# Kernel tuning notes

Measured on AMD Instinct MI355X. Metric: run time of the kernel, lower is better.

The kernel has to match this reference:

```python
import jax, jax.numpy as jnp
import numpy as np

VOCAB = 100000
EMB = 256
HID = 512
HH = HID // 2  # per-direction hidden
NTAGS = 12
START = 10
STOP = 11
SEQ = 2048
NEG = -10000.0


def setup_inputs() -> dict:
    key = jax.random.key(0)
    ks = jax.random.split(key, 18)
    s = 0.05
    inp = {
        "sentence": jax.random.randint(ks[0], (SEQ,), 0, VOCAB, dtype=jnp.int64 if jax.config.jax_enable_x64 else jnp.int32),
        "tags": jax.random.randint(ks[1], (SEQ,), 0, 10, dtype=jnp.int64 if jax.config.jax_enable_x64 else jnp.int32),
        "embed": jax.random.normal(ks[2], (VOCAB, EMB), jnp.float32) * s,
        "Wih_f": jax.random.normal(ks[3], (4 * HH, EMB), jnp.float32) * s,
        "Whh_f": jax.random.normal(ks[4], (4 * HH, HH), jnp.float32) * s,
        "bih_f": jax.random.normal(ks[5], (4 * HH,), jnp.float32) * s,
        "bhh_f": jax.random.normal(ks[6], (4 * HH,), jnp.float32) * s,
        "Wih_b": jax.random.normal(ks[7], (4 * HH, EMB), jnp.float32) * s,
        "Whh_b": jax.random.normal(ks[8], (4 * HH, HH), jnp.float32) * s,
        "bih_b": jax.random.normal(ks[9], (4 * HH,), jnp.float32) * s,
        "bhh_b": jax.random.normal(ks[10], (4 * HH,), jnp.float32) * s,
        "W_out": jax.random.normal(ks[11], (NTAGS, HID), jnp.float32) * s,
        "b_out": jax.random.normal(ks[12], (NTAGS,), jnp.float32) * s,
        "h0": jax.random.normal(ks[14], (2, HH), jnp.float32),
        "c0": jax.random.normal(ks[15], (2, HH), jnp.float32),
    }
    trans = jax.random.normal(ks[13], (NTAGS, NTAGS), jnp.float32)
    trans = trans.at[START, :].set(NEG)  # never transition INTO start
    trans = trans.at[:, STOP].set(NEG)   # never transition FROM stop
    inp["transitions"] = trans
    return inp


def _lstm_dir(x, h0, c0, Wih, Whh, bih, bhh):
    # x: [T, E]; PyTorch gate order i, f, g, o
    pre = x @ Wih.T + bih + bhh  # [T, 4*HH] precomputed input projection
    def step(carry, p):
        h, c = carry
        g = p + Whh @ h
        i, f, gg, o = jnp.split(g, 4)
        i = jax.nn.sigmoid(i)
        f = jax.nn.sigmoid(f)
        gg = jnp.tanh(gg)
        o = jax.nn.sigmoid(o)
        c = f * c + i * gg
        h = o * jnp.tanh(c)
        return (h, c), h
    _, hs = jax.lax.scan(step, (h0, c0), pre)
    return hs  # [T, HH]


def _forward_impl(sentence, tags, embed, Wih_f, Whh_f, bih_f, bhh_f,
                  Wih_b, Whh_b, bih_b, bhh_b, W_out, b_out, transitions, h0, c0):
    x = embed[sentence]  # [T, E]
    hf = _lstm_dir(x, h0[0], c0[0], Wih_f, Whh_f, bih_f, bhh_f)
    hb = jnp.flip(_lstm_dir(jnp.flip(x, 0), h0[1], c0[1], Wih_b, Whh_b, bih_b, bhh_b), 0)
    feats = jnp.concatenate([hf, hb], axis=-1) @ W_out.T + b_out  # [T, NTAGS]

    # CRF forward algorithm: log-semiring scan over time
    fv0 = jnp.full((NTAGS,), NEG, feats.dtype).at[START].set(0.0)
    def crf_step(fv, emit):
        # transitions[next, prev]; logsumexp over prev
        fv = jax.nn.logsumexp(fv[None, :] + transitions + emit[:, None], axis=1)
        return fv, None
    fv, _ = jax.lax.scan(crf_step, fv0, feats)
    forward_score = jax.nn.logsumexp(fv + transitions[STOP])

    # gold path score
    prev = jnp.concatenate([jnp.array([START], dtype=tags.dtype), tags[:-1]])
    emit_gold = jnp.take_along_axis(feats, tags[:, None], axis=1)[:, 0]
    gold_score = jnp.sum(transitions[tags, prev]) + jnp.sum(emit_gold) + transitions[STOP, tags[-1]]

    return forward_score - gold_score


def reference(sentence, tags, embed, Wih_f, Whh_f, bih_f, bhh_f,
              Wih_b, Whh_b, bih_b, bhh_b, W_out, b_out, transitions, h0, c0):
    return _forward_impl(sentence, tags, embed, Wih_f, Whh_f, bih_f, bhh_f,
                         Wih_b, Whh_b, bih_b, bhh_b, W_out, b_out, transitions, h0, c0)
```

## Files before the change

### kernel.cpp

```cpp
#include <hip/hip_runtime.h>
#include <hip/hip_bf16.h>
#include <stdint.h>

#define SEQ   2048
#define EMB   256
#define HHD   256
#define GATES 1024
#define NTAGS 12
#define START 10
#define STOP  11
#define CCH   16
#define CLEN  128

__device__ __forceinline__ int sdot4(uint32_t a, uint32_t b, int c) {
#if __has_builtin(__builtin_amdgcn_sdot4)
  return __builtin_amdgcn_sdot4((int)a, (int)b, c, false);
#else
  int r = c;
#pragma unroll
  for (int i = 0; i < 4; i++) {
    int av = (int)(signed char)((a >> (8 * i)) & 255);
    int bv = (int)(signed char)((b >> (8 * i)) & 255);
    r += av * bv;
  }
  return r;
#endif
}

__device__ __forceinline__ float fsig(float x) {
  float e = __expf(-x);
  return __builtin_amdgcn_rcpf(1.0f + e);
}

__device__ __forceinline__ int dpp_xor1(int x) {
  return __builtin_amdgcn_update_dpp(0, x, 0xB1, 0xF, 0xF, true);
}
__device__ __forceinline__ int dpp_xor2(int x) {
  return __builtin_amdgcn_update_dpp(0, x, 0x4E, 0xF, 0xF, true);
}
__device__ __forceinline__ float dpp_xor2_f(float x) {
  int r = __builtin_amdgcn_update_dpp(0, __float_as_int(x), 0x4E, 0xF, 0xF, true);
  return __int_as_float(r);
}

__global__ __launch_bounds__(256) void k_quant(const float* __restrict__ whh_f,
                                               const float* __restrict__ whh_b,
                                               uint32_t* __restrict__ q4,
                                               float* __restrict__ scales) {
  const int row  = (blockIdx.x * 256 + threadIdx.x) >> 6;
  const int lane = threadIdx.x & 63;
  const int d = row >> 10, r = row & 1023;
  const float4 w = *(const float4*)((d ? whh_b : whh_f) + (long)r * HHD + lane * 4);
  float m = fmaxf(fmaxf(fabsf(w.x), fabsf(w.y)), fmaxf(fabsf(w.z), fabsf(w.w)));
#pragma unroll
  for (int off = 32; off; off >>= 1) m = fmaxf(m, __shfl_xor(m, off, 64));
  m = fmaxf(m, 1e-20f);
  const float inv = 127.f / m;
  int a = (int)rintf(w.x * inv), b = (int)rintf(w.y * inv);
  int c = (int)rintf(w.z * inv), e = (int)rintf(w.w * inv);
  q4[row * 64 + lane] = (uint32_t)(a & 255) | ((uint32_t)(b & 255) << 8) |
                        ((uint32_t)(c & 255) << 16) | ((uint32_t)(e & 255) << 24);
  if (lane == 0) scales[row] = m / 127.f;
}

__global__ __launch_bounds__(256) void k_proj(const int* __restrict__ sentence,
                                              const float* __restrict__ embed,
                                              const float* __restrict__ Wih_f,
                                              const float* __restrict__ bih_f,
                                              const float* __restrict__ bhh_f,
                                              const float* __restrict__ Wih_b,
                                              const float* __restrict__ bih_b,
                                              const float* __restrict__ bhh_b,
                                              float* __restrict__ pre) {
  const int dir = blockIdx.y;
  const int t0  = blockIdx.x * 8;
  const float* Wih = dir ? Wih_b : Wih_f;
  const float* bih = dir ? bih_b : bih_f;
  const float* bhh = dir ? bhh_b : bhh_f;

  __shared__ float xs[8][256];
  const int tid = threadIdx.x;
#pragma unroll
  for (int i = 0; i < 8; i++) {
    int s = sentence[t0 + i];
    xs[i][tid] = embed[(long)s * EMB + tid];
  }
  __syncthreads();

  const int r0 = tid * 4;
  float acc[4][8];
#pragma unroll
  for (int j = 0; j < 4; j++)
#pragma unroll
    for (int t = 0; t < 8; t++) acc[j][t] = 0.f;

  const float4* W4 = (const float4*)Wih;
  for (int kq = 0; kq < 64; kq++) {
    float4 w[4];
#pragma unroll
    for (int j = 0; j < 4; j++) w[j] = W4[(r0 + j) * 64 + kq];
#pragma unroll
    for (int t = 0; t < 8; t++) {
      float4 xv = ((const float4*)xs[t])[kq];
#pragma unroll
      for (int j = 0; j < 4; j++)
        acc[j][t] += w[j].x * xv.x + w[j].y * xv.y + w[j].z * xv.z + w[j].w * xv.w;
    }
  }
#pragma unroll
  for (int j = 0; j < 4; j++) {
    const int row = r0 + j;
    const int G  = row >> 8;
    const int uu = row & 255;
    float bsum = bih[row] + bhh[row];
#pragma unroll
    for (int t = 0; t < 8; t++)
      pre[(((long)(dir * SEQ + t0 + t)) * HHD + uu) * 4 + G] = acc[j][t] + bsum;
  }
}

__global__ __launch_bounds__(512, 2) void k_lstm(const uint32_t* __restrict__ q4,
                                                 const float* __restrict__ scales,
                                                 const float* __restrict__ pre,
                                                 const float* __restrict__ h0,
                                                 const float* __restrict__ c0,
                                                 float* __restrict__ hs) {
  const int dir  = blockIdx.x;
  const int L    = threadIdx.x;
  const int q    = L & 3;
  const int g    = L >> 2;
  const int p    = q & 1;
  const int half = q >> 1;
  const int u    = 2 * g + p;

  __shared__ __align__(16) uint8_t hbuf[2][256];

  const long base = (long)dir * GATES;

  uint4 wa[4][4], wb[4][4];
  const uint4* qq = (const uint4*)q4;
#pragma unroll
  for (int j = 0; j < 4; j++) {
    const int qj = q ^ j;
    const int rA = (2 * (qj >> 1)) * 256 + 2 * g + (qj & 1);
    const int rB = rA + 256;
#pragma unroll
    for (int k = 0; k < 4; k++) {
      wa[j][k] = qq[(base + rA) * 16 + 4 * q + k];
      wb[j][k] = qq[(base + rB) * 16 + 4 * q + k];
    }
  }
  const int rown = (2 * half) * 256 + u;
  const float sA = scales[base + rown];
  const float sB = scales[base + rown + 256];
  const float sA1 = sA * (1.f / 127.f), sA4 = sA * (4.f / 127.f);
  const float sB1 = sB * (1.f / 127.f), sB4 = sB * (4.f / 127.f);

  if (L < 256) {
    float v = h0[dir * HHD + L] * (127.f / 4.f);
    v = fminf(fmaxf(v, -127.f), 127.f);
    hbuf[0][L] = (uint8_t)(int)rintf(v);
  }
  float c_st = c0[dir * HHD + u];
  __syncthreads();

  const int t0 = dir ? (SEQ - 1) : 0;
  const long pstep = dir ? -(long)(HHD * 4) : (long)(HHD * 4);
  const long hstep = dir ? -(long)HHD : (long)HHD;
  const float* pp = pre + (long)dir * SEQ * (HHD * 4) + ((long)t0 * HHD + u) * 4 + 2 * half;
  float* hp       = hs  + (long)dir * SEQ * HHD + (long)t0 * HHD + u;
  const float gmul = half ? 2.f : 1.f;
  const int write_h = ((L & 2) == 0);

  float2 pr = *(const float2*)pp;

  for (int s = 0; s < SEQ; s++) {
#pragma unroll
    for (int j = 0; j < 4; j++)
#pragma unroll
      for (int k = 0; k < 4; k++) {
        asm volatile("" : "+v"(wa[j][k].x), "+v"(wa[j][k].y),
                          "+v"(wa[j][k].z), "+v"(wa[j][k].w));
        asm volatile("" : "+v"(wb[j][k].x), "+v"(wb[j][k].y),
                          "+v"(wb[j][k].z), "+v"(wb[j][k].w));
      }

    pp += pstep;
    const float2 prn = *(const float2*)pp;

    const uint4* hq4 = (const uint4*)(hbuf[s & 1] + (q << 6));
    const uint4 h0v = hq4[0], h1v = hq4[1], h2v = hq4[2], h3v = hq4[3];

    int pa0 = 0, pa1 = 0, pa2 = 0, pa3 = 0;
    int pb0 = 0, pb1 = 0, pb2 = 0, pb3 = 0;
#pragma unroll
    for (int k = 0; k < 4; k++) {
      const uint4 hk = (k == 0) ? h0v : (k == 1) ? h1v : (k == 2) ? h2v : h3v;
      pa0 = sdot4(wa[0][k].x, hk.x, pa0); pa0 = sdot4(wa[0][k].y, hk.y, pa0);
      pa0 = sdot4(wa[0][k].z, hk.z, pa0); pa0 = sdot4(wa[0][k].w, hk.w, pa0);
      pa1 = sdot4(wa[1][k].x, hk.x, pa1); pa1 = sdot4(wa[1][k].y, hk.y, pa1);
      pa1 = sdot4(wa[1][k].z, hk.z, pa1); pa1 = sdot4(wa[1][k].w, hk.w, pa1);
      pa2 = sdot4(wa[2][k].x, hk.x, pa2); pa2 = sdot4(wa[2][k].y, hk.y, pa2);
      pa2 = sdot4(wa[2][k].z, hk.z, pa2); pa2 = sdot4(wa[2][k].w, hk.w, pa2);
      pa3 = sdot4(wa[3][k].x, hk.x, pa3); pa3 = sdot4(wa[3][k].y, hk.y, pa3);
      pa3 = sdot4(wa[3][k].z, hk.z, pa3); pa3 = sdot4(wa[3][k].w, hk.w, pa3);
      pb0 = sdot4(wb[0][k].x, hk.x, pb0); pb0 = sdot4(wb[0][k].y, hk.y, pb0);
      pb0 = sdot4(wb[0][k].z, hk.z, pb0); pb0 = sdot4(wb[0][k].w, hk.w, pb0);
      pb1 = sdot4(wb[1][k].x, hk.x, pb1); pb1 = sdot4(wb[1][k].y, hk.y, pb1);
      pb1 = sdot4(wb[1][k].z, hk.z, pb1); pb1 = sdot4(wb[1][k].w, hk.w, pb1);
      pb2 = sdot4(wb[2][k].x, hk.x, pb2); pb2 = sdot4(wb[2][k].y, hk.y, pb2);
      pb2 = sdot4(wb[2][k].z, hk.z, pb2); pb2 = sdot4(wb[2][k].w, hk.w, pb2);
      pb3 = sdot4(wb[3][k].x, hk.x, pb3); pb3 = sdot4(wb[3][k].y, hk.y, pb3);
      pb3 = sdot4(wb[3][k].z, hk.z, pb3); pb3 = sdot4(wb[3][k].w, hk.w, pb3);
    }
    const int tA = pa0 + dpp_xor1(pa1);
    const int tA2 = pa2 + dpp_xor1(pa3);
    const int sumA = tA + dpp_xor2(tA2);
    const int tB = pb0 + dpp_xor1(pb1);
    const int tB2 = pb2 + dpp_xor1(pb3);
    const int sumB = tB + dpp_xor2(tB2);

    const float sAh = s ? sA1 : sA4;
    const float sBh = s ? sB1 : sB4;
    const float gA = fmaf(sAh, (float)sumA, pr.x);
    const float gB = fmaf(sBh, (float)sumB, pr.y);

    const float v0 = fsig(gA * gmul) * gmul - (gmul - 1.f);
    const float v1 = fsig(gB);
    const float p0 = dpp_xor2_f(v0);
    const float p1 = dpp_xor2_f(v1);
    const float iv = half ? p0 : v0;
    const float fv = half ? p1 : v1;
    const float gv = half ? v0 : p0;
    const float ov = half ? v1 : p1;

    c_st = fv * c_st + iv * gv;
    const float hv = ov * (2.f * fsig(2.f * c_st) - 1.f);

    if (write_h) {
      *hp = hv;
      hbuf[(s + 1) & 1][u] = (uint8_t)(int)rintf(hv * 127.f);
    }
    pr = prn;
    hp += hstep;
    asm volatile("s_waitcnt lgkmcnt(0)\n\ts_barrier" ::: "memory");
  }
}

__global__ __launch_bounds__(192) void k_feats(const float* __restrict__ hs,
                                               const float* __restrict__ W_out,
                                               const float* __restrict__ b_out,
                                               float* __restrict__ feats) {
  __shared__ float Wl[12 * 520];
  const int tid = threadIdx.x;
  for (int i = tid; i < 12 * 512; i += 192) Wl[(i / 512) * 520 + (i % 512)] = W_out[i];
  __syncthreads();

  const int tl = tid / 12, n = tid % 12;
  const int t = blockIdx.x * 16 + tl;
  const float4* hf4 = (const float4*)(hs + (long)t * HHD);
  const float4* hb4 = (const float4*)(hs + (long)SEQ * HHD + (long)t * HHD);
  const float4* Wa  = (const float4*)&Wl[n * 520];
  const float4* Wb  = (const float4*)&Wl[n * 520 + 256];

  float acc = b_out[n];
#pragma unroll 8
  for (int j = 0; j < 64; j++) {
    float4 w = Wa[j], h = hf4[j];
    acc += w.x * h.x + w.y * h.y + w.z * h.z + w.w * h.w;
  }
#pragma unroll 8
  for (int j = 0; j < 64; j++) {
    float4 w = Wb[j], h = hb4[j];
    acc += w.x * h.x + w.y * h.y + w.z * h.z + w.w * h.w;
  }
  feats[t * NTAGS + n] = acc;
}

__global__ __launch_bounds__(192) void k_crf_chunk(const float* __restrict__ feats,
                                                   const float* __restrict__ trans,
                                                   float* __restrict__ Pc) {
  const int ch  = blockIdx.x;
  const int tid = threadIdx.x;
  const int n   = tid & 15;
  const int p   = tid >> 4;
  const int nn  = (n < 12) ? n : 11;

  __shared__ float fe[CLEN * NTAGS];
  for (int i = tid; i < CLEN * NTAGS; i += 192) fe[i] = feats[ch * CLEN * NTAGS + i];
  __syncthreads();

  float trn[12];
#pragma unroll
  for (int j = 0; j < 12; j++) trn[j] = trans[nn * 12 + j];

  float Mv = trans[nn * 12 + p] + fe[nn];
  for (int t = 1; t < CLEN; t++) {
    float x[12], m = -1e30f;
#pragma unroll
    for (int j = 0; j < 12; j++) {
      x[j] = trn[j] + __shfl(Mv, (tid & 48) | j, 64);
      m = fmaxf(m, x[j]);
    }
    float ss = 0.f;
#pragma unroll
    for (int j = 0; j < 12; j++) ss += __expf(x[j] - m);
    Mv = fe[t * NTAGS + nn] + m + __logf(ss);
  }
  if (n < 12) Pc[ch * 144 + n * 12 + p] = Mv;
}

__global__ __launch_bounds__(128) void k_crf_final(const float* __restrict__ Pc,
                                                   const float* __restrict__ feats,
                                                   const int* __restrict__ tags,
                                                   const float* __restrict__ trans,
                                                   float* __restrict__ out) {
  __shared__ float Pl[CCH * 144];
  __shared__ float res[2];
  const int tid = threadIdx.x;
  for (int i = tid; i < CCH * 144; i += 128) Pl[i] = Pc[i];
  __syncthreads();

  if (tid < 64) {
    const int n  = tid;
    const int nn = (n < 12) ? n : 11;
    float fv = (n == START) ? 0.f : -10000.f;
    for (int c = 0; c < CCH; c++) {
      float x[12], m = -1e30f;
#pragma unroll
      for (int j = 0; j < 12; j++) {
        x[j] = Pl[c * 144 + nn * 12 + j] + __shfl(fv, j, 64);
        m = fmaxf(m, x[j]);
      }
      float ss = 0.f;
#pragma unroll
      for (int j = 0; j < 12; j++) ss += __expf(x[j] - m);
      fv = m + __logf(ss);
    }
    const float v = fv + trans[STOP * 12 + nn];
    float xs[12], m = -1e30f;
#pragma unroll
    for (int j = 0; j < 12; j++) {
      xs[j] = __shfl(v, j, 64);
      m = fmaxf(m, xs[j]);
    }
    float ss = 0.f;
#pragma unroll
    for (int j = 0; j < 12; j++) ss += __expf(xs[j] - m);
    if (tid == 0) res[0] = m + __logf(ss);
  } else {
    const int i = tid - 64;
    float gp = 0.f;
    for (int b = 0; b < 32; b++) {
      int t  = b * 64 + i;
      int tg = tags[t];
      int pv = (t == 0) ? START : tags[t - 1];
      gp += trans[tg * 12 + pv] + feats[t * NTAGS + tg];
    }
#pragma unroll
    for (int off = 32; off; off >>= 1) gp += __shfl_xor(gp, off, 64);
    if (i == 0) res[1] = gp + trans[STOP * 12 + tags[SEQ - 1]];
  }
  __syncthreads();
  if (tid == 0) out[0] = res[0] - res[1];
}

extern "C" void kernel_launch(void* const* d_in, const int* in_sizes, int n_in,
                              void* d_out, int out_size, void* d_ws, size_t ws_size,
                              hipStream_t stream) {
  const int*   sentence = (const int*)  d_in[0];
  const int*   tags     = (const int*)  d_in[1];
  const float* embed    = (const float*)d_in[2];
  const float* Wih_f    = (const float*)d_in[3];
  const float* Whh_f    = (const float*)d_in[4];
  const float* bih_f    = (const float*)d_in[5];
  const float* bhh_f    = (const float*)d_in[6];
  const float* Wih_b    = (const float*)d_in[7];
  const float* Whh_b    = (const float*)d_in[8];
  const float* bih_b    = (const float*)d_in[9];
  const float* bhh_b    = (const float*)d_in[10];
  const float* W_out    = (const float*)d_in[11];
  const float* b_out    = (const float*)d_in[12];
  const float* h0       = (const float*)d_in[13];
  const float* c0       = (const float*)d_in[14];
  const float* trans    = (const float*)d_in[15];
  float* out = (float*)d_out;

  char* ws = (char*)d_ws;
  uint32_t* q4    = (uint32_t*)ws;
  float*    scales= (float*)(ws + (512l << 10));
  float*    pre   = (float*)(ws + (1l  << 20));
  float*    hs    = (float*)(ws + (17l << 20));
  float*    feats = (float*)(ws + (21l << 20));
  float*    Pc    = (float*)(ws + (21l << 20) + (128l<<10));

  k_quant<<<512, 256, 0, stream>>>(Whh_f, Whh_b, q4, scales);
  k_proj<<<dim3(256, 2), 256, 0, stream>>>(sentence, embed, Wih_f, bih_f, bhh_f,
                                           Wih_b, bih_b, bhh_b, pre);
  k_lstm<<<2, 512, 0, stream>>>(q4, scales, pre, h0, c0, hs);
  k_feats<<<128, 192, 0, stream>>>(hs, W_out, b_out, feats);
  k_crf_chunk<<<CCH, 192, 0, stream>>>(feats, trans, Pc);
  k_crf_final<<<1, 128, 0, stream>>>(Pc, feats, tags, trans, out);
}
```

Measured before the change: 2.035 ms.

## Double LSTM block to 1024 threads with per-unit quad work split

The recurrent LSTM kernel now runs 1024 threads per direction. Four lanes serve each hidden unit: two split the K dimension in halves and two hold different gate pairs, so each thread keeps 16 uint4 weight registers instead of 32 and reduces with a single DPP xor1. The asm register pins are dropped and the inline barrier becomes __syncthreads. Each thread does less dot-product work per step, but the barrier now spans twice as many waves and the old 2-waves-per-SIMD occupancy hint is gone.

```diff
diff --git a/kernel.cpp b/kernel.cpp
--- a/kernel.cpp
+++ b/kernel.cpp
@@ -34,9 +34,6 @@
 
 __device__ __forceinline__ int dpp_xor1(int x) {
   return __builtin_amdgcn_update_dpp(0, x, 0xB1, 0xF, 0xF, true);
-}
-__device__ __forceinline__ int dpp_xor2(int x) {
-  return __builtin_amdgcn_update_dpp(0, x, 0x4E, 0xF, 0xF, true);
 }
 __device__ __forceinline__ float dpp_xor2_f(float x) {
   int r = __builtin_amdgcn_update_dpp(0, __float_as_int(x), 0x4E, 0xF, 0xF, true);
@@ -119,40 +116,34 @@
   }
 }
 
-__global__ __launch_bounds__(512, 2) void k_lstm(const uint32_t* __restrict__ q4,
-                                                 const float* __restrict__ scales,
-                                                 const float* __restrict__ pre,
-                                                 const float* __restrict__ h0,
-                                                 const float* __restrict__ c0,
-                                                 float* __restrict__ hs) {
+__global__ __launch_bounds__(1024) void k_lstm(const uint32_t* __restrict__ q4,
+                                               const float* __restrict__ scales,
+                                               const float* __restrict__ pre,
+                                               const float* __restrict__ h0,
+                                               const float* __restrict__ c0,
+                                               float* __restrict__ hs) {
   const int dir  = blockIdx.x;
   const int L    = threadIdx.x;
   const int q    = L & 3;
-  const int g    = L >> 2;
-  const int p    = q & 1;
+  const int u    = L >> 2;
+  const int kh   = q & 1;
   const int half = q >> 1;
-  const int u    = 2 * g + p;
 
   __shared__ __align__(16) uint8_t hbuf[2][256];
 
+  const int rowA = half * 512 + u;
+  const int rowB = rowA + 256;
   const long base = (long)dir * GATES;
 
-  uint4 wa[4][4], wb[4][4];
+  uint4 wA[8], wB[8];
   const uint4* qq = (const uint4*)q4;
 #pragma unroll
-  for (int j = 0; j < 4; j++) {
-    const int qj = q ^ j;
-    const int rA = (2 * (qj >> 1)) * 256 + 2 * g + (qj & 1);
-    const int rB = rA + 256;
-#pragma unroll
-    for (int k = 0; k < 4; k++) {
-      wa[j][k] = qq[(base + rA) * 16 + 4 * q + k];
-      wb[j][k] = qq[(base + rB) * 16 + 4 * q + k];
-    }
-  }
-  const int rown = (2 * half) * 256 + u;
-  const float sA = scales[base + rown];
-  const float sB = scales[base + rown + 256];
+  for (int j = 0; j < 8; j++) {
+    wA[j] = qq[(base + rowA) * 16 + kh * 8 + j];
+    wB[j] = qq[(base + rowB) * 16 + kh * 8 + j];
+  }
+  const float sA = scales[base + rowA];
+  const float sB = scales[base + rowB];
   const float sA1 = sA * (1.f / 127.f), sA4 = sA * (4.f / 127.f);
   const float sB1 = sB * (1.f / 127.f), sB4 = sB * (4.f / 127.f);
 
@@ -170,55 +161,42 @@
   const float* pp = pre + (long)dir * SEQ * (HHD * 4) + ((long)t0 * HHD + u) * 4 + 2 * half;
   float* hp       = hs  + (long)dir * SEQ * HHD + (long)t0 * HHD + u;
   const float gmul = half ? 2.f : 1.f;
-  const int write_h = ((L & 2) == 0);
+  const int writer = (q == 0);
 
   float2 pr = *(const float2*)pp;
 
   for (int s = 0; s < SEQ; s++) {
-#pragma unroll
-    for (int j = 0; j < 4; j++)
-#pragma unroll
-      for (int k = 0; k < 4; k++) {
-        asm volatile("" : "+v"(wa[j][k].x), "+v"(wa[j][k].y),
-                          "+v"(wa[j][k].z), "+v"(wa[j][k].w));
-        asm volatile("" : "+v"(wb[j][k].x), "+v"(wb[j][k].y),
-                          "+v"(wb[j][k].z), "+v"(wb[j][k].w));
-      }
-
     pp += pstep;
     const float2 prn = *(const float2*)pp;
 
-    const uint4* hq4 = (const uint4*)(hbuf[s & 1] + (q << 6));
-    const uint4 h0v = hq4[0], h1v = hq4[1], h2v = hq4[2], h3v = hq4[3];
-
-    int pa0 = 0, pa1 = 0, pa2 = 0, pa3 = 0;
-    int pb0 = 0, pb1 = 0, pb2 = 0, pb3 = 0;
-#pragma unroll
-    for (int k = 0; k < 4; k++) {
-      const uint4 hk = (k == 0) ? h0v : (k == 1) ? h1v : (k == 2) ? h2v : h3v;
-      pa0 = sdot4(wa[0][k].x, hk.x, pa0); pa0 = sdot4(wa[0][k].y, hk.y, pa0);
-      pa0 = sdot4(wa[0][k].z, hk.z, pa0); pa0 = sdot4(wa[0][k].w, hk.w, pa0);
-      pa1 = sdot4(wa[1][k].x, hk.x, pa1); pa1 = sdot4(wa[1][k].y, hk.y, pa1);
-      pa1 = sdot4(wa[1][k].z, hk.z, pa1); pa1 = sdot4(wa[1][k].w, hk.w, pa1);
-      pa2 = sdot4(wa[2][k].x, hk.x, pa2); pa2 = sdot4(wa[2][k].y, hk.y, pa2);
-      pa2 = sdot4(wa[2][k].z, hk.z, pa2); pa2 = sdot4(wa[2][k].w, hk.w, pa2);
-      pa3 = sdot4(wa[3][k].x, hk.x, pa3); pa3 = sdot4(wa[3][k].y, hk.y, pa3);
-      pa3 = sdot4(wa[3][k].z, hk.z, pa3); pa3 = sdot4(wa[3][k].w, hk.w, pa3);
-      pb0 = sdot4(wb[0][k].x, hk.x, pb0); pb0 = sdot4(wb[0][k].y, hk.y, pb0);
-      pb0 = sdot4(wb[0][k].z, hk.z, pb0); pb0 = sdot4(wb[0][k].w, hk.w, pb0);
-      pb1 = sdot4(wb[1][k].x, hk.x, pb1); pb1 = sdot4(wb[1][k].y, hk.y, pb1);
-      pb1 = sdot4(wb[1][k].z, hk.z, pb1); pb1 = sdot4(wb[1][k].w, hk.w, pb1);
-      pb2 = sdot4(wb[2][k].x, hk.x, pb2); pb2 = sdot4(wb[2][k].y, hk.y, pb2);
-      pb2 = sdot4(wb[2][k].z, hk.z, pb2); pb2 = sdot4(wb[2][k].w, hk.w, pb2);
-      pb3 = sdot4(wb[3][k].x, hk.x, pb3); pb3 = sdot4(wb[3][k].y, hk.y, pb3);
-      pb3 = sdot4(wb[3][k].z, hk.z, pb3); pb3 = sdot4(wb[3][k].w, hk.w, pb3);
-    }
-    const int tA = pa0 + dpp_xor1(pa1);
-    const int tA2 = pa2 + dpp_xor1(pa3);
-    const int sumA = tA + dpp_xor2(tA2);
-    const int tB = pb0 + dpp_xor1(pb1);
-    const int tB2 = pb2 + dpp_xor1(pb3);
-    const int sumB = tB + dpp_xor2(tB2);
+    const uint4* hq4 = (const uint4*)(hbuf[s & 1] + (kh << 7));
+
+    int a0 = 0, a1 = 0, b0 = 0, b1 = 0;
+    {
+      uint4 hh[4];
+#pragma unroll
+      for (int j = 0; j < 4; j++) hh[j] = hq4[j];
+#pragma unroll
+      for (int j = 0; j < 4; j++) {
+        a0 = sdot4(wA[j].x, hh[j].x, a0); a1 = sdot4(wA[j].y, hh[j].y, a1);
+        a0 = sdot4(wA[j].z, hh[j].z, a0); a1 = sdot4(wA[j].w, hh[j].w, a1);
+        b0 = sdot4(wB[j].x, hh[j].x, b0); b1 = sdot4(wB[j].y, hh[j].y, b1);
+        b0 = sdot4(wB[j].z, hh[j].z, b0); b1 = sdot4(wB[j].w, hh[j].w, b1);
+      }
+#pragma unroll
+      for (int j = 0; j < 4; j++) hh[j] = hq4[4 + j];
+#pragma unroll
+      for (int j = 0; j < 4; j++) {
+        a0 = sdot4(wA[4 + j].x, hh[j].x, a0); a1 = sdot4(wA[4 + j].y, hh[j].y, a1);
+        a0 = sdot4(wA[4 + j].z, hh[j].z, a0); a1 = sdot4(wA[4 + j].w, hh[j].w, a1);
+        b0 = sdot4(wB[4 + j].x, hh[j].x, b0); b1 = sdot4(wB[4 + j].y, hh[j].y, b1);
+        b0 = sdot4(wB[4 + j].z, hh[j].z, b0); b1 = sdot4(wB[4 + j].w, hh[j].w, b1);
+      }
+    }
+    const int aP = a0 + a1;
+    const int bP = b0 + b1;
+    const int sumA = aP + dpp_xor1(aP);
+    const int sumB = bP + dpp_xor1(bP);
 
     const float sAh = s ? sA1 : sA4;
     const float sBh = s ? sB1 : sB4;
@@ -237,13 +215,13 @@
     c_st = fv * c_st + iv * gv;
     const float hv = ov * (2.f * fsig(2.f * c_st) - 1.f);
 
-    if (write_h) {
+    if (writer) {
       *hp = hv;
       hbuf[(s + 1) & 1][u] = (uint8_t)(int)rintf(hv * 127.f);
     }
     pr = prn;
     hp += hstep;
-    asm volatile("s_waitcnt lgkmcnt(0)\n\ts_barrier" ::: "memory");
+    __syncthreads();
   }
 }
 
@@ -397,7 +375,7 @@
   k_quant<<<512, 256, 0, stream>>>(Whh_f, Whh_b, q4, scales);
   k_proj<<<dim3(256, 2), 256, 0, stream>>>(sentence, embed, Wih_f, bih_f, bhh_f,
                                            Wih_b, bih_b, bhh_b, pre);
-  k_lstm<<<2, 512, 0, stream>>>(q4, scales, pre, h0, c0, hs);
+  k_lstm<<<2, 1024, 0, stream>>>(q4, scales, pre, h0, c0, hs);
   k_feats<<<128, 192, 0, stream>>>(hs, W_out, b_out, feats);
   k_crf_chunk<<<CCH, 192, 0, stream>>>(feats, trans, Pc);
   k_crf_final<<<1, 128, 0, stream>>>(Pc, feats, tags, trans, out);
```

Result: slower. 2.165 ms (+6.4%).
